# Kernel optimization log

Measured on AMD Instinct MI355X. Metric: run time of the kernel, lower is better.

Reference implementation:

```python
import jax, jax.numpy as jnp
import numpy as np

TEMPERATURE = 0.07
SIM_THRESHOLD = 0.5


def setup_inputs() -> dict:
    key = jax.random.key(0)
    k1, k2 = jax.random.split(key)
    features = jax.random.normal(k1, (4096, 2, 128), dtype=jnp.float32)
    labels = jax.random.randint(k2, (4096, 100), 0, 2).astype(jnp.float32)
    return {"features": features, "labels": labels}


def reference(features, labels):
    B, V, D = features.shape

    # label Jaccard similarity -> positive/negative masks [B, B]
    intersection = labels @ labels.T
    row_sum = jnp.sum(labels, axis=1, keepdims=True)
    union = row_sum + row_sum.T - intersection
    similarity = intersection / (union + 1e-6)
    positive_mask = (similarity >= SIM_THRESHOLD).astype(jnp.float32)
    negative_mask = 1.0 - positive_mask

    # torch.cat(torch.unbind(features, dim=1), dim=0) -> [V*B, D] (view-major)
    contrast_feature = jnp.transpose(features, (1, 0, 2)).reshape(V * B, D)
    dot_similarities = (contrast_feature @ contrast_feature.T) / TEMPERATURE  # [VB, VB]

    # numerical stability: subtract detached row max over the FULL row
    logits_max = jax.lax.stop_gradient(jnp.max(dot_similarities, axis=1, keepdims=True))
    logits = dot_similarities - logits_max

    # only the top-left [B, B] block is ever indexed by the original loop
    e = jnp.exp(logits[:B, :B])
    pos_sum = jnp.sum(e * positive_mask, axis=1)  # [B]
    neg_sum = jnp.sum(e * negative_mask, axis=1)  # [B]

    has_pos = jnp.sum(positive_mask, axis=1) > 0  # rows with >=1 positive
    pos_safe = jnp.where(has_pos, pos_sum, 1.0)
    den_safe = jnp.where(has_pos, pos_sum + neg_sum, 1.0)
    per_row = -jnp.log(pos_safe / den_safe)

    count = jnp.sum(has_pos.astype(jnp.float32))
    loss = jnp.sum(jnp.where(has_pos, per_row, 0.0)) / jnp.maximum(count, 1.0)
    return loss
```

## Files before the change

### kernel.cpp

```cpp
#include <hip/hip_runtime.h>
#include <math.h>

#define B_ROWS 4096
#define NVIEW 2
#define DIM 128
#define LBL 100
#define VB 8192
#define NCHUNK 16
#define CHUNK 512

typedef __attribute__((ext_vector_type(8))) short bf16x8;
typedef __attribute__((ext_vector_type(4))) float f32x4;

__device__ __forceinline__ unsigned short f2bf(float x) {
  union { float f; unsigned u; } a; a.f = x;
  unsigned r = a.u + 0x7fffu + ((a.u >> 16) & 1u);
  return (unsigned short)(r >> 16);
}

__global__ void zero_kernel(float* accum) {
  if (threadIdx.x < 2) accum[threadIdx.x] = 0.0f;
}

__global__ void pack_kernel(const float* __restrict__ feat,
                            const float* __restrict__ labels,
                            unsigned short* __restrict__ cfA,
                            unsigned short* __restrict__ cfB,
                            uint4* __restrict__ Lb,
                            int* __restrict__ rsv) {
  const float invT = 1.0f / 0.07f;
  int w = (int)((blockIdx.x * blockDim.x + threadIdx.x) >> 6);
  int lane = threadIdx.x & 63;
  if (w >= VB) return;
  int b = w & (B_ROWS - 1);
  int v = w >> 12;
  const float2* src = (const float2*)(feat + ((size_t)b * NVIEW + v) * DIM);
  float2 f = src[lane];
  ((unsigned*)(cfB + (size_t)w * DIM))[lane] =
      (unsigned)f2bf(f.x) | ((unsigned)f2bf(f.y) << 16);
  if (v == 0) {
    ((unsigned*)(cfA + (size_t)w * DIM))[lane] =
        (unsigned)f2bf(f.x * invT) | ((unsigned)f2bf(f.y * invT) << 16);
    float x0 = labels[(size_t)w * LBL + lane];
    float x1 = (lane < LBL - 64) ? labels[(size_t)w * LBL + 64 + lane] : 0.0f;
    unsigned long long b0 = __ballot(x0 != 0.0f);
    unsigned long long b1 = __ballot(x1 != 0.0f);
    if (lane == 0) {
      Lb[w] = make_uint4((unsigned)b0, (unsigned)(b0 >> 32),
                         (unsigned)b1, (unsigned)(b1 >> 32));
      rsv[w] = __popcll(b0) + __popcll(b1);
    }
  }
}

__launch_bounds__(256, 2)
__global__ void main_kernel(const unsigned short* __restrict__ cfA,
                            const unsigned short* __restrict__ cfB,
                            const uint4* __restrict__ Lb,
                            const int* __restrict__ rsv,
                            float4* __restrict__ part) {
  __shared__ uint4 As[2048];
  __shared__ uint4 Bs[2048];
  const int tid = threadIdx.x;
  const int lane = tid & 63;
  const int wave = tid >> 6;
  const int l15 = lane & 15;
  const int quad = lane >> 4;
  const int wi = (wave & 1) * 64;
  const int wj = (wave >> 1) * 64;
  const int rowBase = blockIdx.x * 128;
  const int chunkBase = blockIdx.y * CHUNK;
  const bool maskRegion = (chunkBase < B_ROWS);

  {
    const uint4* srcA = (const uint4*)(cfA + (size_t)rowBase * DIM);
    #pragma unroll
    for (int it = 0; it < 8; ++it) {
      int flat = it * 256 + tid;
      int r = flat >> 4, kc = flat & 15;
      As[kc * 128 + (r ^ kc)] = srcA[flat];
    }
  }

  float m_s[16], p_s[16], n_s[16];
  #pragma unroll
  for (int i = 0; i < 16; ++i) { m_s[i] = -INFINITY; p_s[i] = 0.f; n_s[i] = 0.f; }

  const bf16x8* Asv = (const bf16x8*)As;
  const bf16x8* Bsv = (const bf16x8*)Bs;

  for (int jt = 0; jt < 4; ++jt) {
    const int colBase = chunkBase + jt * 128;
    __syncthreads();
    {
      const uint4* srcB = (const uint4*)(cfB + (size_t)colBase * DIM);
      #pragma unroll
      for (int it = 0; it < 8; ++it) {
        int flat = it * 256 + tid;
        int r = flat >> 4, kc = flat & 15;
        Bs[kc * 128 + (r ^ kc)] = srcB[flat];
      }
    }
    __syncthreads();

    f32x4 acc[4][4];
    #pragma unroll
    for (int ti = 0; ti < 4; ++ti)
      #pragma unroll
      for (int tj = 0; tj < 4; ++tj)
        acc[ti][tj] = (f32x4){0.f, 0.f, 0.f, 0.f};

    #pragma unroll
    for (int ks = 0; ks < 4; ++ks) {
      const int kc = ks * 4 + quad;
      const int abase = kc * 128 + wi + (l15 ^ kc);
      const int bbase = kc * 128 + wj + (l15 ^ kc);
      bf16x8 af[4], bfr[4];
      #pragma unroll
      for (int t = 0; t < 4; ++t) {
        af[t] = Asv[abase + t * 16];
        bfr[t] = Bsv[bbase + t * 16];
      }
      #pragma unroll
      for (int ti = 0; ti < 4; ++ti)
        #pragma unroll
        for (int tj = 0; tj < 4; ++tj)
          acc[ti][tj] = __builtin_amdgcn_mfma_f32_16x16x32_bf16(
              af[ti], bfr[tj], acc[ti][tj], 0, 0, 0);
    }

    if (!maskRegion) {
      #pragma unroll
      for (int ti = 0; ti < 4; ++ti)
        #pragma unroll
        for (int r = 0; r < 4; ++r) {
          float tm = fmaxf(fmaxf(acc[ti][0][r], acc[ti][1][r]),
                           fmaxf(acc[ti][2][r], acc[ti][3][r]));
          int si = ti * 4 + r;
          m_s[si] = fmaxf(m_s[si], tm);
        }
    } else {
      #pragma unroll
      for (int ti = 0; ti < 4; ++ti)
        #pragma unroll
        for (int r = 0; r < 4; ++r) {
          int si = ti * 4 + r;
          float l0 = acc[ti][0][r], l1 = acc[ti][1][r];
          float l2 = acc[ti][2][r], l3 = acc[ti][3][r];
          float tm = fmaxf(fmaxf(l0, l1), fmaxf(l2, l3));
          float m = m_s[si];
          if (tm > m - 90.0f) {
            int grow = rowBase + wi + ti * 16 + quad * 4 + r;
            uint4 la = Lb[grow];
            int ra = rsv[grow];
            float newm = fmaxf(m, tm);
            float sc = __expf(m - newm);
            float p = p_s[si] * sc, n = n_s[si] * sc;
            float lv[4] = {l0, l1, l2, l3};
            #pragma unroll
            for (int tj = 0; tj < 4; ++tj) {
              float e = __expf(lv[tj] - newm);
              int gcol = colBase + wj + tj * 16 + l15;
              uint4 lb = Lb[gcol];
              int rb = rsv[gcol];
              int inter = __popc(la.x & lb.x) + __popc(la.y & lb.y) +
                          __popc(la.z & lb.z) + __popc(la.w & lb.w);
              if (3 * inter > ra + rb) p += e; else n += e;
            }
            m_s[si] = newm; p_s[si] = p; n_s[si] = n;
          }
        }
    }
  }

  #pragma unroll
  for (int si = 0; si < 16; ++si) {
    float m = m_s[si], p = p_s[si], n = n_s[si];
    #pragma unroll
    for (int off = 8; off >= 1; off >>= 1) {
      float om = __shfl_xor(m, off);
      float op = __shfl_xor(p, off);
      float on = __shfl_xor(n, off);
      float nm = fmaxf(m, om);
      float s0 = __expf(m - nm), s1 = __expf(om - nm);
      p = p * s0 + op * s1;
      n = n * s0 + on * s1;
      m = nm;
    }
    m_s[si] = m; p_s[si] = p; n_s[si] = n;
  }

  __syncthreads();
  float* mbuf = (float*)As;
  if (wj == 64 && l15 == 0) {
    #pragma unroll
    for (int ti = 0; ti < 4; ++ti)
      #pragma unroll
      for (int r = 0; r < 4; ++r) {
        int row = wi + ti * 16 + quad * 4 + r;
        int si = ti * 4 + r;
        mbuf[row * 3 + 0] = m_s[si];
        mbuf[row * 3 + 1] = p_s[si];
        mbuf[row * 3 + 2] = n_s[si];
      }
  }
  __syncthreads();
  if (wj == 0 && l15 == 0) {
    #pragma unroll
    for (int ti = 0; ti < 4; ++ti)
      #pragma unroll
      for (int r = 0; r < 4; ++r) {
        int row = wi + ti * 16 + quad * 4 + r;
        int si = ti * 4 + r;
        float m = m_s[si], p = p_s[si], n = n_s[si];
        float om = mbuf[row * 3 + 0], op = mbuf[row * 3 + 1], on = mbuf[row * 3 + 2];
        float nm = fmaxf(m, om);
        float s0 = __expf(m - nm), s1 = __expf(om - nm);
        p = p * s0 + op * s1;
        n = n * s0 + on * s1;
        part[(size_t)blockIdx.y * B_ROWS + rowBase + row] = make_float4(nm, p, n, 0.f);
      }
  }
}

__global__ void merge_kernel(const float4* __restrict__ part,
                             const int* __restrict__ rsv,
                             float* __restrict__ accum) {
  int row = blockIdx.x * blockDim.x + threadIdx.x;
  float M = -INFINITY;
  #pragma unroll
  for (int c = 0; c < NCHUNK; ++c)
    M = fmaxf(M, part[(size_t)c * B_ROWS + row].x);
  float p = 0.f, n = 0.f;
  #pragma unroll
  for (int c = 0; c < NCHUNK; ++c) {
    float4 v = part[(size_t)c * B_ROWS + row];
    float s = __expf(v.x - M);
    p += v.y * s;
    n += v.z * s;
  }
  bool has = rsv[row] > 0;
  float per = has ? -logf(p / (p + n)) : 0.f;
  float cnt = has ? 1.f : 0.f;
  #pragma unroll
  for (int off = 32; off >= 1; off >>= 1) {
    per += __shfl_xor(per, off);
    cnt += __shfl_xor(cnt, off);
  }
  if ((threadIdx.x & 63) == 0) {
    atomicAdd(accum + 0, per);
    atomicAdd(accum + 1, cnt);
  }
}

__global__ void fin_kernel(const float* __restrict__ accum, float* __restrict__ out) {
  out[0] = accum[0] / fmaxf(accum[1], 1.0f);
}

extern "C" void kernel_launch(void* const* d_in, const int* in_sizes, int n_in,
                              void* d_out, int out_size, void* d_ws, size_t ws_size,
                              hipStream_t stream) {
  const float* feat = (const float*)d_in[0];
  const float* labels = (const float*)d_in[1];
  float* out = (float*)d_out;
  char* ws = (char*)d_ws;
  float* accum = (float*)(ws + 0);
  int* rsv = (int*)(ws + 16);
  uint4* Lbm = (uint4*)(ws + 16 + 16384);
  unsigned short* cfA = (unsigned short*)(ws + 81952);
  unsigned short* cfB = (unsigned short*)(ws + 81952 + 1048576);
  float4* part = (float4*)(ws + 81952 + 1048576 + 2097152);

  hipLaunchKernelGGL(zero_kernel, dim3(1), dim3(64), 0, stream, accum);
  hipLaunchKernelGGL(pack_kernel, dim3(VB / 4), dim3(256), 0, stream,
                     feat, labels, cfA, cfB, Lbm, rsv);
  hipLaunchKernelGGL(main_kernel, dim3(32, NCHUNK), dim3(256), 0, stream,
                     cfA, cfB, Lbm, rsv, part);
  hipLaunchKernelGGL(merge_kernel, dim3(B_ROWS / 256), dim3(256), 0, stream,
                     part, rsv, accum);
  hipLaunchKernelGGL(fin_kernel, dim3(1), dim3(1), 0, stream, accum, out);
}
```

Baseline: 97.75 us.

## Seed row max with self-similarity, hoist column label loads, fold zero kernel

The pack kernel now computes each row's bf16 self dot product (a near-maximum of the row) and stores it as an initial running max, so the main kernel's online softmax starts from a high max and skips the rescale branch for most tiles. Column label bitmasks and row sums are loaded once per column tile instead of inside the per-row inner loop. The separate zero kernel is folded into the pack kernel, removing one launch. The seed minus a margin assumes the self-similarity is close to the true row max, which may not hold for other inputs, and the hoisted label loads add registers in a kernel already bounded by launch_bounds.

```diff
diff --git a/kernel.cpp b/kernel.cpp
--- a/kernel.cpp
+++ b/kernel.cpp
@@ -18,17 +18,16 @@
   return (unsigned short)(r >> 16);
 }
 
-__global__ void zero_kernel(float* accum) {
-  if (threadIdx.x < 2) accum[threadIdx.x] = 0.0f;
-}
-
 __global__ void pack_kernel(const float* __restrict__ feat,
                             const float* __restrict__ labels,
                             unsigned short* __restrict__ cfA,
                             unsigned short* __restrict__ cfB,
                             uint4* __restrict__ Lb,
-                            int* __restrict__ rsv) {
+                            int* __restrict__ rsv,
+                            float* __restrict__ seedv,
+                            float* __restrict__ accum) {
   const float invT = 1.0f / 0.07f;
+  if (blockIdx.x == 0 && threadIdx.x < 2) accum[threadIdx.x] = 0.0f;
   int w = (int)((blockIdx.x * blockDim.x + threadIdx.x) >> 6);
   int lane = threadIdx.x & 63;
   if (w >= VB) return;
@@ -36,11 +35,15 @@
   int v = w >> 12;
   const float2* src = (const float2*)(feat + ((size_t)b * NVIEW + v) * DIM);
   float2 f = src[lane];
-  ((unsigned*)(cfB + (size_t)w * DIM))[lane] =
-      (unsigned)f2bf(f.x) | ((unsigned)f2bf(f.y) << 16);
+  unsigned ub0 = f2bf(f.x), ub1 = f2bf(f.y);
+  ((unsigned*)(cfB + (size_t)w * DIM))[lane] = ub0 | (ub1 << 16);
   if (v == 0) {
-    ((unsigned*)(cfA + (size_t)w * DIM))[lane] =
-        (unsigned)f2bf(f.x * invT) | ((unsigned)f2bf(f.y * invT) << 16);
+    unsigned ua0 = f2bf(f.x * invT), ua1 = f2bf(f.y * invT);
+    ((unsigned*)(cfA + (size_t)w * DIM))[lane] = ua0 | (ua1 << 16);
+    float s = __uint_as_float(ua0 << 16) * __uint_as_float(ub0 << 16) +
+              __uint_as_float(ua1 << 16) * __uint_as_float(ub1 << 16);
+    #pragma unroll
+    for (int off = 32; off >= 1; off >>= 1) s += __shfl_xor(s, off);
     float x0 = labels[(size_t)w * LBL + lane];
     float x1 = (lane < LBL - 64) ? labels[(size_t)w * LBL + 64 + lane] : 0.0f;
     unsigned long long b0 = __ballot(x0 != 0.0f);
@@ -49,6 +52,7 @@
       Lb[w] = make_uint4((unsigned)b0, (unsigned)(b0 >> 32),
                          (unsigned)b1, (unsigned)(b1 >> 32));
       rsv[w] = __popcll(b0) + __popcll(b1);
+      seedv[w] = s - 2.0f;
     }
   }
 }
@@ -58,6 +62,7 @@
                             const unsigned short* __restrict__ cfB,
                             const uint4* __restrict__ Lb,
                             const int* __restrict__ rsv,
+                            const float* __restrict__ seedv,
                             float4* __restrict__ part) {
   __shared__ uint4 As[2048];
   __shared__ uint4 Bs[2048];
@@ -84,7 +89,13 @@
 
   float m_s[16], p_s[16], n_s[16];
   #pragma unroll
-  for (int i = 0; i < 16; ++i) { m_s[i] = -INFINITY; p_s[i] = 0.f; n_s[i] = 0.f; }
+  for (int ti = 0; ti < 4; ++ti)
+    #pragma unroll
+    for (int r = 0; r < 4; ++r) {
+      m_s[ti * 4 + r] = seedv[rowBase + wi + ti * 16 + quad * 4 + r];
+      p_s[ti * 4 + r] = 0.f;
+      n_s[ti * 4 + r] = 0.f;
+    }
 
   const bf16x8* Asv = (const bf16x8*)As;
   const bf16x8* Bsv = (const bf16x8*)Bs;
@@ -102,6 +113,17 @@
       }
     }
     __syncthreads();
+
+    uint4 clb[4];
+    int crs[4];
+    if (maskRegion) {
+      #pragma unroll
+      for (int tj = 0; tj < 4; ++tj) {
+        int gcol = colBase + wj + tj * 16 + l15;
+        clb[tj] = Lb[gcol];
+        crs[tj] = rsv[gcol];
+      }
+    }
 
     f32x4 acc[4][4];
     #pragma unroll
@@ -160,12 +182,9 @@
             #pragma unroll
             for (int tj = 0; tj < 4; ++tj) {
               float e = __expf(lv[tj] - newm);
-              int gcol = colBase + wj + tj * 16 + l15;
-              uint4 lb = Lb[gcol];
-              int rb = rsv[gcol];
-              int inter = __popc(la.x & lb.x) + __popc(la.y & lb.y) +
-                          __popc(la.z & lb.z) + __popc(la.w & lb.w);
-              if (3 * inter > ra + rb) p += e; else n += e;
+              int inter = __popc(la.x & clb[tj].x) + __popc(la.y & clb[tj].y) +
+                          __popc(la.z & clb[tj].z) + __popc(la.w & clb[tj].w);
+              if (3 * inter > ra + crs[tj]) p += e; else n += e;
             }
             m_s[si] = newm; p_s[si] = p; n_s[si] = n;
           }
@@ -270,12 +289,12 @@
   unsigned short* cfA = (unsigned short*)(ws + 81952);
   unsigned short* cfB = (unsigned short*)(ws + 81952 + 1048576);
   float4* part = (float4*)(ws + 81952 + 1048576 + 2097152);
-
-  hipLaunchKernelGGL(zero_kernel, dim3(1), dim3(64), 0, stream, accum);
+  float* seedv = (float*)(ws + 81952 + 1048576 + 2097152 + 1048576);
+
   hipLaunchKernelGGL(pack_kernel, dim3(VB / 4), dim3(256), 0, stream,
-                     feat, labels, cfA, cfB, Lbm, rsv);
+                     feat, labels, cfA, cfB, Lbm, rsv, seedv, accum);
   hipLaunchKernelGGL(main_kernel, dim3(32, NCHUNK), dim3(256), 0, stream,
-                     cfA, cfB, Lbm, rsv, part);
+                     cfA, cfB, Lbm, rsv, seedv, part);
   hipLaunchKernelGGL(merge_kernel, dim3(B_ROWS / 256), dim3(256), 0, stream,
                      part, rsv, accum);
   hipLaunchKernelGGL(fin_kernel, dim3(1), dim3(1), 0, stream, accum, out);
```

Result: faster. 85.05 us (-13.0%).
